# Kernel optimization log

Measured on AMD Instinct MI355X. Metric: run time of the kernel, lower is better.

Reference implementation:

```python
import jax, jax.numpy as jnp
import numpy as np

B, N, E = 16, 64, 512
C_IMG = 512
H1, H2, H3 = 256, 128, 64
U, R = 8, 8
BBC = 9
EH1, EH2 = 64, 64
BBOX_POS_MAX = 1024.0
EPS = 1e-5


def setup_inputs():
    key = jax.random.key(0)
    ks = jax.random.split(key, 24)
    f = lambda i, shape, s=0.05: jax.random.normal(ks[i], shape, jnp.float32) * s
    return {
        'roi_features': f(0, (B, N, C_IMG), 1.0),
        'batch_bboxes': jax.random.uniform(ks[1], (B, N, 4)) * BBOX_POS_MAX,
        'batch_directions': jax.random.uniform(ks[2], (B, N, 4)),
        'batch_priorities': jax.random.uniform(ks[3], (B, N)),
        'w1': f(4, (C_IMG, H1)), 'b1': f(5, (H1,)),
        'bn1_g': jnp.ones((H1,)), 'bn1_b': jnp.zeros((H1,)),
        'bn1_m': jnp.zeros((H1,)), 'bn1_v': jnp.ones((H1,)),
        'w2': f(6, (H1, H2)), 'b2': f(7, (H2,)),
        'bn2_g': jnp.ones((H2,)), 'bn2_b': jnp.zeros((H2,)),
        'bn2_m': jnp.zeros((H2,)), 'bn2_v': jnp.ones((H2,)),
        'w3': f(8, (H2, H3)), 'b3': f(9, (H3,)),
        'wn': f(10, (H3, U)), 'bn_c': f(11, (U,)),
        'we1': f(12, (2 * BBC, EH1)), 'be1': f(13, (EH1,)),
        'we2': f(14, (EH1, EH2)), 'be2': f(15, (EH2,)),
        'wei': f(16, (EH2, R)), 'bei': f(17, (R,)),
        'edge_index': jax.random.randint(ks[18], (B, 2, E), 0, N, dtype=jnp.int32),
    }


def _bn(x, g, b, m, v):
    # BatchNorm1d in eval mode (running stats)
    return (x - m) * jax.lax.rsqrt(v + EPS) * g + b


def _build_see(edge_index):
    # Padded neighbor table replacing edge_index2dict:
    # see[b,n,0] = n, then srcs of edges with dst==n, in original edge order.
    src = edge_index[:, 0, :]                                   # [B,E]
    dst = edge_index[:, 1, :]                                   # [B,E]
    eq = dst[:, :, None] == dst[:, None, :]                     # [B,E,E]
    lower = jnp.tril(jnp.ones((E, E), bool), -1)
    pos = jnp.sum(eq & lower, axis=-1) + 1                      # rank within dst group, +1 for self slot
    see = jnp.zeros((B, N, N), jnp.int32).at[:, :, 0].set(jnp.arange(N, dtype=jnp.int32))
    b_idx = jnp.arange(B)[:, None]
    see = see.at[b_idx, dst, pos].set(src, mode='drop')
    deg = jnp.zeros((B, N), jnp.int32).at[b_idx, dst].add(1)
    count = jnp.minimum(deg + 1, N)
    mask = (jnp.arange(N)[None, None, :] < count[:, :, None]).astype(jnp.float32)  # [B,N,N]
    return see, mask


def _forward(roi_features, batch_bboxes, batch_directions, batch_priorities,
             w1, b1, bn1_g, bn1_b, bn1_m, bn1_v,
             w2, b2, bn2_g, bn2_b, bn2_m, bn2_v,
             w3, b3, wn, bn_c,
             we1, be1, we2, be2, wei, bei, edge_index):
    see, mask = _build_see(edge_index)
    # --- node branch (node_predictor + node_concept_interpreter) ---
    x = roi_features.reshape(B * N, C_IMG)
    x = jax.nn.relu(_bn(x @ w1 + b1, bn1_g, bn1_b, bn1_m, bn1_v))
    x = jax.nn.relu(_bn(x @ w2 + b2, bn2_g, bn2_b, bn2_m, bn2_v))
    x = jax.nn.relu(x @ w3 + b3)
    node_c = jax.nn.sigmoid(x @ wn + bn_c).reshape(B, N, U)
    # get_nlm_unary_concepts: gather per-node neighborhood into dense [B,N,N,U]
    gu = jax.vmap(lambda u, s: u[s])(node_c, see)               # [B,N,N,U]
    node_concepts = (gu * mask[..., None]).reshape(B * N, N, U)
    # --- edge branch ---
    attr = jnp.concatenate([batch_bboxes / BBOX_POS_MAX, batch_directions,
                            batch_priorities[..., None]], axis=-1)  # [B,N,BBC]
    pair = jnp.concatenate([
        jnp.broadcast_to(attr[:, :, None, :], (B, N, N, BBC)),
        jnp.broadcast_to(attr[:, None, :, :], (B, N, N, BBC))], axis=-1).reshape(-1, 2 * BBC)
    e = jax.nn.relu(pair @ we1 + be1)
    e = jax.nn.relu(e @ we2 + be2)
    rel = jax.nn.sigmoid(e @ wei + bei).reshape(B, N, N, R)
    # get_nlm_binary_concepts: rel[b, see[b,n,i], see[b,n,j]] with zero padding
    def per_b(r, s, m):
        g = r[s[:, :, None], s[:, None, :]]                     # [N,N,N,R]
        return g * (m[:, :, None, None] * m[:, None, :, None])
    edge_concepts = jax.vmap(per_b)(rel, see, mask).reshape(B * N, N, N, R)
    return node_concepts, edge_concepts


def reference(roi_features, batch_bboxes, batch_directions, batch_priorities,
              w1, b1, bn1_g, bn1_b, bn1_m, bn1_v,
              w2, b2, bn2_g, bn2_b, bn2_m, bn2_v,
              w3, b3, wn, bn_c,
              we1, be1, we2, be2, wei, bei, edge_index):
    return _forward(roi_features, batch_bboxes, batch_directions, batch_priorities,
                    w1, b1, bn1_g, bn1_b, bn1_m, bn1_v,
                    w2, b2, bn2_g, bn2_b, bn2_m, bn2_v,
                    w3, b3, wn, bn_c,
                    we1, be1, we2, be2, wei, bei, edge_index)
```

## Files before the change

### kernel.cpp

```cpp
#include <hip/hip_runtime.h>
#include <math.h>

#define BB    16
#define NN    64
#define EE    512
#define CIMG  512
#define H1D   256
#define H2D   128
#define H3D   64
#define UD    8
#define RD    8
#define BBCD  9
#define EH1D  64
#define EH2D  64
#define EPSF  1e-5f

typedef float nfloat4 __attribute__((ext_vector_type(4)));

__global__ __launch_bounds__(256) void prep_node_kernel(
    const int* __restrict__ edge_index,
    const float* __restrict__ bboxes,
    const float* __restrict__ dirs,
    const float* __restrict__ prios,
    const float* __restrict__ we1,
    const float* __restrict__ be1,
    int* __restrict__ see, int* __restrict__ cnt,
    float* __restrict__ P, float* __restrict__ Q,
    const float* __restrict__ roi,
    const float* __restrict__ w1, const float* __restrict__ b1,
    const float* __restrict__ g1, const float* __restrict__ bt1,
    const float* __restrict__ m1, const float* __restrict__ v1,
    const float* __restrict__ w2, const float* __restrict__ b2,
    const float* __restrict__ g2, const float* __restrict__ bt2,
    const float* __restrict__ m2, const float* __restrict__ v2,
    const float* __restrict__ w3, const float* __restrict__ b3,
    const float* __restrict__ wn, const float* __restrict__ bnc,
    float* __restrict__ node_c)
{
    __shared__ union {
        struct {
            int src[EE];
            int dst[EE];
            int see[NN * NN];
            float attr[NN][BBCD];
        } p;
        struct {
            float h1[4][H1D];
            float h2[4][H2D];
            float h3[4][H3D];
        } n;
    } sm;

    const int t = threadIdx.x;

    if (blockIdx.x < BB) {
        const int b = blockIdx.x;
        const int* ei = edge_index + b * 2 * EE;
        for (int e = t; e < EE; e += 256) {
            sm.p.src[e] = ei[e];
            sm.p.dst[e] = ei[EE + e];
        }
        for (int x = t; x < NN * NN; x += 256)
            sm.p.see[x] = ((x & (NN - 1)) == 0) ? (x >> 6) : 0;
        if (t < NN) {
            const float* bbp = bboxes + (b * NN + t) * 4;
            const float* ddp = dirs + (b * NN + t) * 4;
            sm.p.attr[t][0] = bbp[0] * (1.0f / 1024.0f);
            sm.p.attr[t][1] = bbp[1] * (1.0f / 1024.0f);
            sm.p.attr[t][2] = bbp[2] * (1.0f / 1024.0f);
            sm.p.attr[t][3] = bbp[3] * (1.0f / 1024.0f);
            sm.p.attr[t][4] = ddp[0];
            sm.p.attr[t][5] = ddp[1];
            sm.p.attr[t][6] = ddp[2];
            sm.p.attr[t][7] = ddp[3];
            sm.p.attr[t][8] = prios[b * NN + t];
        }
        __syncthreads();

        if (t < NN) {
            int pos = 0;
            #pragma unroll 8
            for (int e = 0; e < EE; ++e) {
                if (sm.p.dst[e] == t) {
                    ++pos;
                    if (pos < NN) sm.p.see[t * NN + pos] = sm.p.src[e];
                }
            }
            int c = pos + 1;
            cnt[b * NN + t] = (c < NN) ? c : NN;
        }
        __syncthreads();

        {
            int4* dst4 = (int4*)(see + b * NN * NN);
            const int4* src4 = (const int4*)sm.p.see;
            for (int x = t; x < (NN * NN) / 4; x += 256) dst4[x] = src4[x];
        }

        for (int x = t; x < NN * EH1D; x += 256) {
            int n = x >> 6, o = x & 63;
            float p = 0.f;
            float q = be1[o];
            #pragma unroll
            for (int c = 0; c < BBCD; ++c) {
                float a = sm.p.attr[n][c];
                p = fmaf(a, we1[c * EH1D + o], p);
                q = fmaf(a, we1[(BBCD + c) * EH1D + o], q);
            }
            P[(b * NN + n) * EH1D + o] = p;
            Q[(b * NN + n) * EH1D + o] = q;
        }
        return;
    }

    const int row0 = (blockIdx.x - BB) * 4;

    {
        const int og = t & 63, rg = t >> 6;
        const int o0 = og * 4;
        const float4* xrow = (const float4*)(roi + (size_t)(row0 + rg) * CIMG);
        float a0 = 0.f, a1 = 0.f, a2 = 0.f, a3 = 0.f;
        for (int cg = 0; cg < CIMG / 4; ++cg) {
            float4 xv = xrow[cg];
            float4 wv0 = ((const float4*)(w1 + (size_t)(cg * 4 + 0) * H1D))[og];
            float4 wv1 = ((const float4*)(w1 + (size_t)(cg * 4 + 1) * H1D))[og];
            float4 wv2 = ((const float4*)(w1 + (size_t)(cg * 4 + 2) * H1D))[og];
            float4 wv3 = ((const float4*)(w1 + (size_t)(cg * 4 + 3) * H1D))[og];
            a0 = fmaf(xv.x, wv0.x, a0); a1 = fmaf(xv.x, wv0.y, a1);
            a2 = fmaf(xv.x, wv0.z, a2); a3 = fmaf(xv.x, wv0.w, a3);
            a0 = fmaf(xv.y, wv1.x, a0); a1 = fmaf(xv.y, wv1.y, a1);
            a2 = fmaf(xv.y, wv1.z, a2); a3 = fmaf(xv.y, wv1.w, a3);
            a0 = fmaf(xv.z, wv2.x, a0); a1 = fmaf(xv.z, wv2.y, a1);
            a2 = fmaf(xv.z, wv2.z, a2); a3 = fmaf(xv.z, wv2.w, a3);
            a0 = fmaf(xv.w, wv3.x, a0); a1 = fmaf(xv.w, wv3.y, a1);
            a2 = fmaf(xv.w, wv3.z, a2); a3 = fmaf(xv.w, wv3.w, a3);
        }
        float4 bv = ((const float4*)b1)[og];
        float4 gv = ((const float4*)g1)[og];
        float4 btv = ((const float4*)bt1)[og];
        float4 mv = ((const float4*)m1)[og];
        float4 vv = ((const float4*)v1)[og];
        float s0 = rsqrtf(vv.x + EPSF) * gv.x;
        float s1 = rsqrtf(vv.y + EPSF) * gv.y;
        float s2 = rsqrtf(vv.z + EPSF) * gv.z;
        float s3 = rsqrtf(vv.w + EPSF) * gv.w;
        sm.n.h1[rg][o0 + 0] = fmaxf(0.f, (a0 + bv.x - mv.x) * s0 + btv.x);
        sm.n.h1[rg][o0 + 1] = fmaxf(0.f, (a1 + bv.y - mv.y) * s1 + btv.y);
        sm.n.h1[rg][o0 + 2] = fmaxf(0.f, (a2 + bv.z - mv.z) * s2 + btv.z);
        sm.n.h1[rg][o0 + 3] = fmaxf(0.f, (a3 + bv.w - mv.w) * s3 + btv.w);
    }
    __syncthreads();

    if (t < 128) {
        const int og = t & 31, rg = t >> 5;
        const int o0 = og * 4;
        const float4* xrow = (const float4*)&sm.n.h1[rg][0];
        float a0 = 0.f, a1 = 0.f, a2 = 0.f, a3 = 0.f;
        for (int cg = 0; cg < H1D / 4; ++cg) {
            float4 xv = xrow[cg];
            float4 wv0 = ((const float4*)(w2 + (size_t)(cg * 4 + 0) * H2D))[og];
            float4 wv1 = ((const float4*)(w2 + (size_t)(cg * 4 + 1) * H2D))[og];
            float4 wv2 = ((const float4*)(w2 + (size_t)(cg * 4 + 2) * H2D))[og];
            float4 wv3 = ((const float4*)(w2 + (size_t)(cg * 4 + 3) * H2D))[og];
            a0 = fmaf(xv.x, wv0.x, a0); a1 = fmaf(xv.x, wv0.y, a1);
            a2 = fmaf(xv.x, wv0.z, a2); a3 = fmaf(xv.x, wv0.w, a3);
            a0 = fmaf(xv.y, wv1.x, a0); a1 = fmaf(xv.y, wv1.y, a1);
            a2 = fmaf(xv.y, wv1.z, a2); a3 = fmaf(xv.y, wv1.w, a3);
            a0 = fmaf(xv.z, wv2.x, a0); a1 = fmaf(xv.z, wv2.y, a1);
            a2 = fmaf(xv.z, wv2.z, a2); a3 = fmaf(xv.z, wv2.w, a3);
            a0 = fmaf(xv.w, wv3.x, a0); a1 = fmaf(xv.w, wv3.y, a1);
            a2 = fmaf(xv.w, wv3.z, a2); a3 = fmaf(xv.w, wv3.w, a3);
        }
        float4 bv = ((const float4*)b2)[og];
        float4 gv = ((const float4*)g2)[og];
        float4 btv = ((const float4*)bt2)[og];
        float4 mv = ((const float4*)m2)[og];
        float4 vv = ((const float4*)v2)[og];
        float s0 = rsqrtf(vv.x + EPSF) * gv.x;
        float s1 = rsqrtf(vv.y + EPSF) * gv.y;
        float s2 = rsqrtf(vv.z + EPSF) * gv.z;
        float s3 = rsqrtf(vv.w + EPSF) * gv.w;
        sm.n.h2[rg][o0 + 0] = fmaxf(0.f, (a0 + bv.x - mv.x) * s0 + btv.x);
        sm.n.h2[rg][o0 + 1] = fmaxf(0.f, (a1 + bv.y - mv.y) * s1 + btv.y);
        sm.n.h2[rg][o0 + 2] = fmaxf(0.f, (a2 + bv.z - mv.z) * s2 + btv.z);
        sm.n.h2[rg][o0 + 3] = fmaxf(0.f, (a3 + bv.w - mv.w) * s3 + btv.w);
    }
    __syncthreads();

    if (t < 64) {
        const int og = t & 15, rg = t >> 4;
        const int o0 = og * 4;
        const float4* xrow = (const float4*)&sm.n.h2[rg][0];
        float a0 = 0.f, a1 = 0.f, a2 = 0.f, a3 = 0.f;
        #pragma unroll 4
        for (int cg = 0; cg < H2D / 4; ++cg) {
            float4 xv = xrow[cg];
            float4 wv0 = ((const float4*)(w3 + (size_t)(cg * 4 + 0) * H3D))[og];
            float4 wv1 = ((const float4*)(w3 + (size_t)(cg * 4 + 1) * H3D))[og];
            float4 wv2 = ((const float4*)(w3 + (size_t)(cg * 4 + 2) * H3D))[og];
            float4 wv3 = ((const float4*)(w3 + (size_t)(cg * 4 + 3) * H3D))[og];
            a0 = fmaf(xv.x, wv0.x, a0); a1 = fmaf(xv.x, wv0.y, a1);
            a2 = fmaf(xv.x, wv0.z, a2); a3 = fmaf(xv.x, wv0.w, a3);
            a0 = fmaf(xv.y, wv1.x, a0); a1 = fmaf(xv.y, wv1.y, a1);
            a2 = fmaf(xv.y, wv1.z, a2); a3 = fmaf(xv.y, wv1.w, a3);
            a0 = fmaf(xv.z, wv2.x, a0); a1 = fmaf(xv.z, wv2.y, a1);
            a2 = fmaf(xv.z, wv2.z, a2); a3 = fmaf(xv.z, wv2.w, a3);
            a0 = fmaf(xv.w, wv3.x, a0); a1 = fmaf(xv.w, wv3.y, a1);
            a2 = fmaf(xv.w, wv3.z, a2); a3 = fmaf(xv.w, wv3.w, a3);
        }
        float4 bv = ((const float4*)b3)[og];
        sm.n.h3[rg][o0 + 0] = fmaxf(0.f, a0 + bv.x);
        sm.n.h3[rg][o0 + 1] = fmaxf(0.f, a1 + bv.y);
        sm.n.h3[rg][o0 + 2] = fmaxf(0.f, a2 + bv.z);
        sm.n.h3[rg][o0 + 3] = fmaxf(0.f, a3 + bv.w);
    }
    __syncthreads();

    if (t < 32) {
        const int o = t & 7, r = t >> 3;
        float a = bnc[o];
        #pragma unroll 8
        for (int c = 0; c < H3D; ++c) a = fmaf(sm.n.h3[r][c], wn[c * UD + o], a);
        node_c[(size_t)(row0 + r) * UD + o] = 1.f / (1.f + expf(-a));
    }
}

__global__ __launch_bounds__(256) void edge_zero_kernel(
    const float* __restrict__ P, const float* __restrict__ Q,
    const float* __restrict__ we2, const float* __restrict__ be2,
    const float* __restrict__ wei, const float* __restrict__ bei,
    const int* __restrict__ cnt,
    float* __restrict__ rel, float* __restrict__ out_edge)
{
    __shared__ float e1_s[NN * 68];
    __shared__ float qw_s[NN * EH1D];
    __shared__ float wei_s[EH2D * RD];
    __shared__ float Pi_s[EH1D];
    __shared__ float be2_s[EH2D];
    __shared__ float bei_s[RD];

    const int t = threadIdx.x;
    const int id = blockIdx.x >> 1;

    if ((blockIdx.x & 1) == 0) {
        const int c = cnt[id];
        float* outb = out_edge + (size_t)id * NN * NN * RD;
        const nfloat4 z = {0.f, 0.f, 0.f, 0.f};
        #pragma unroll
        for (int it = 0; it < (NN * NN) / 256; ++it) {
            int task = it * 256 + t;
            int j = task >> 6, k = task & 63;
            if (j >= c || k >= c) {
                nfloat4* dst = (nfloat4*)(outb + (size_t)task * RD);
                __builtin_nontemporal_store(z, dst);
                __builtin_nontemporal_store(z, dst + 1);
            }
        }
        return;
    }

    const int b = id >> 6;
    const int i = id & 63;

    {
        const float4* Qb4 = (const float4*)(Q + (size_t)b * NN * EH1D);
        float4* qw4 = (float4*)qw_s;
        #pragma unroll
        for (int x = 0; x < 4; ++x) qw4[x * 256 + t] = Qb4[x * 256 + t];
        if (t < EH1D) Pi_s[t] = P[(size_t)(b * NN + i) * EH1D + t];
        if (t < 128) ((float4*)wei_s)[t] = ((const float4*)wei)[t];
        if (t < EH2D) be2_s[t] = be2[t];
        if (t < RD) bei_s[t] = bei[t];
    }
    __syncthreads();

    {
        const int j = t & 63, cg = t >> 6;
        const float4* qrow = (const float4*)(qw_s + j * EH1D);
        const float4* prow = (const float4*)Pi_s;
        #pragma unroll
        for (int q = 0; q < 4; ++q) {
            int c4 = cg * 4 + q;
            float4 qv = qrow[c4];
            float4 pv = prow[c4];
            float4 ev;
            ev.x = fmaxf(0.f, qv.x + pv.x);
            ev.y = fmaxf(0.f, qv.y + pv.y);
            ev.z = fmaxf(0.f, qv.z + pv.z);
            ev.w = fmaxf(0.f, qv.w + pv.w);
            *(float4*)(e1_s + j * 68 + c4 * 4) = ev;
        }
    }
    __syncthreads();

    {
        const float4* w4 = (const float4*)we2;
        float4* qw4 = (float4*)qw_s;
        #pragma unroll
        for (int x = 0; x < 4; ++x) qw4[x * 256 + t] = w4[x * 256 + t];
    }
    __syncthreads();

    const int tx = t & 15, ty = t >> 4;
    const int o0 = tx * 4, j0 = ty * 4;
    float acc[4][4];
    #pragma unroll
    for (int r = 0; r < 4; ++r)
        #pragma unroll
        for (int o = 0; o < 4; ++o) acc[r][o] = 0.f;

    #pragma unroll 4
    for (int cg = 0; cg < 16; ++cg) {
        float ev[4][4];
        #pragma unroll
        for (int r = 0; r < 4; ++r) {
            float4 v = *(const float4*)(e1_s + (j0 + r) * 68 + cg * 4);
            ev[r][0] = v.x; ev[r][1] = v.y; ev[r][2] = v.z; ev[r][3] = v.w;
        }
        #pragma unroll
        for (int q = 0; q < 4; ++q) {
            float4 wv = *(const float4*)(qw_s + (cg * 4 + q) * EH1D + o0);
            #pragma unroll
            for (int r = 0; r < 4; ++r) {
                acc[r][0] = fmaf(ev[r][q], wv.x, acc[r][0]);
                acc[r][1] = fmaf(ev[r][q], wv.y, acc[r][1]);
                acc[r][2] = fmaf(ev[r][q], wv.z, acc[r][2]);
                acc[r][3] = fmaf(ev[r][q], wv.w, acc[r][3]);
            }
        }
    }

    {
        float4 bv = *(const float4*)(be2_s + o0);
        #pragma unroll
        for (int r = 0; r < 4; ++r) {
            float4 v;
            v.x = fmaxf(0.f, acc[r][0] + bv.x);
            v.y = fmaxf(0.f, acc[r][1] + bv.y);
            v.z = fmaxf(0.f, acc[r][2] + bv.z);
            v.w = fmaxf(0.f, acc[r][3] + bv.w);
            *(float4*)(e1_s + (j0 + r) * 68 + o0) = v;
        }
    }
    __syncthreads();

    {
        const int j = t >> 2;
        const int r0 = (t & 3) * 2;
        float a0 = bei_s[r0], a1 = bei_s[r0 + 1];
        const float* e2row = e1_s + j * 68;
        #pragma unroll
        for (int og = 0; og < 16; ++og) {
            float4 e2v = *(const float4*)(e2row + og * 4);
            float2 w0 = *(const float2*)(wei_s + (og * 4 + 0) * RD + r0);
            float2 w1 = *(const float2*)(wei_s + (og * 4 + 1) * RD + r0);
            float2 w2 = *(const float2*)(wei_s + (og * 4 + 2) * RD + r0);
            float2 w3 = *(const float2*)(wei_s + (og * 4 + 3) * RD + r0);
            a0 = fmaf(e2v.x, w0.x, a0); a1 = fmaf(e2v.x, w0.y, a1);
            a0 = fmaf(e2v.y, w1.x, a0); a1 = fmaf(e2v.y, w1.y, a1);
            a0 = fmaf(e2v.z, w2.x, a0); a1 = fmaf(e2v.z, w2.y, a1);
            a0 = fmaf(e2v.w, w3.x, a0); a1 = fmaf(e2v.w, w3.y, a1);
        }
        float2 o;
        o.x = 1.f / (1.f + expf(-a0));
        o.y = 1.f / (1.f + expf(-a1));
        *(float2*)(rel + ((size_t)(b * NN + i) * NN + j) * RD + r0) = o;
    }
}

__global__ __launch_bounds__(256) void gather_kernel(
    const int* __restrict__ see, const int* __restrict__ cnt,
    const float* __restrict__ node_c, const float* __restrict__ rel,
    float* __restrict__ out_node, float* __restrict__ out_edge)
{
    __shared__ int s_s[NN];

    const int t = threadIdx.x;
    const int bi = blockIdx.x;
    const int b = bi >> 6;
    const int c = cnt[bi];

    if (t < NN) s_s[t] = see[bi * NN + t];
    __syncthreads();

    if (t < NN) {
        const float m = (t < c) ? 1.f : 0.f;
        const float4* src = (const float4*)(node_c + (size_t)(b * NN + s_s[t]) * UD);
        float4 v0 = src[0], v1 = src[1];
        v0.x *= m; v0.y *= m; v0.z *= m; v0.w *= m;
        v1.x *= m; v1.y *= m; v1.z *= m; v1.w *= m;
        float4* dst = (float4*)(out_node + ((size_t)bi * NN + t) * UD);
        dst[0] = v0;
        dst[1] = v1;
    }

    const float* relb = rel + (size_t)b * NN * NN * RD;
    float* outb = out_edge + (size_t)bi * NN * NN * RD;

    const int total = c * c;
    for (int task = t; task < total; task += 256) {
        int j = task / c;
        int k = task - j * c;
        const float4* src =
            (const float4*)(relb + (size_t)(s_s[j] * NN + s_s[k]) * RD);
        float4 v0 = src[0], v1 = src[1];
        float4* dst = (float4*)(outb + ((size_t)j * NN + k) * RD);
        dst[0] = v0;
        dst[1] = v1;
    }
}

extern "C" void kernel_launch(void* const* d_in, const int* in_sizes, int n_in,
                              void* d_out, int out_size, void* d_ws, size_t ws_size,
                              hipStream_t stream)
{
    const float* roi  = (const float*)d_in[0];
    const float* bbox = (const float*)d_in[1];
    const float* dirs = (const float*)d_in[2];
    const float* prio = (const float*)d_in[3];
    const float* w1   = (const float*)d_in[4];
    const float* b1   = (const float*)d_in[5];
    const float* g1   = (const float*)d_in[6];
    const float* bt1  = (const float*)d_in[7];
    const float* m1   = (const float*)d_in[8];
    const float* v1   = (const float*)d_in[9];
    const float* w2   = (const float*)d_in[10];
    const float* b2   = (const float*)d_in[11];
    const float* g2   = (const float*)d_in[12];
    const float* bt2  = (const float*)d_in[13];
    const float* m2   = (const float*)d_in[14];
    const float* v2   = (const float*)d_in[15];
    const float* w3   = (const float*)d_in[16];
    const float* b3   = (const float*)d_in[17];
    const float* wn   = (const float*)d_in[18];
    const float* bnc  = (const float*)d_in[19];
    const float* we1  = (const float*)d_in[20];
    const float* be1  = (const float*)d_in[21];
    const float* we2  = (const float*)d_in[22];
    const float* be2  = (const float*)d_in[23];
    const float* wei  = (const float*)d_in[24];
    const float* bei  = (const float*)d_in[25];
    const int* edge_index = (const int*)d_in[26];

    char* ws = (char*)d_ws;
    int*   see    = (int*)ws;   ws += (size_t)BB * NN * NN * 4;
    int*   cnt    = (int*)ws;   ws += (size_t)BB * NN * 4;
    float* Pbuf   = (float*)ws; ws += (size_t)BB * NN * EH1D * 4;
    float* Qbuf   = (float*)ws; ws += (size_t)BB * NN * EH1D * 4;
    float* node_c = (float*)ws; ws += (size_t)BB * NN * UD * 4;
    float* rel    = (float*)ws; ws += (size_t)BB * NN * NN * RD * 4;

    float* out_node = (float*)d_out;
    float* out_edge = (float*)d_out + (size_t)BB * NN * NN * UD;

    hipLaunchKernelGGL(prep_node_kernel, dim3(BB + 256), dim3(256), 0, stream,
                       edge_index, bbox, dirs, prio, we1, be1,
                       see, cnt, Pbuf, Qbuf,
                       roi, w1, b1, g1, bt1, m1, v1,
                       w2, b2, g2, bt2, m2, v2,
                       w3, b3, wn, bnc, node_c);
    hipLaunchKernelGGL(edge_zero_kernel, dim3(2 * BB * NN), dim3(256), 0, stream,
                       Pbuf, Qbuf, we2, be2, wei, bei, cnt, rel, out_edge);
    hipLaunchKernelGGL(gather_kernel, dim3(BB * NN), dim3(256), 0, stream,
                       see, cnt, node_c, rel, out_node, out_edge);
}
```

Measured before the change: 283.7 us.

## Register-tile node MLP with split-K reduction and move edge zeroing into first kernel

The node MLP layers now use 4x4 register tiles per thread with split-K partial sums reduced through shared memory. This replaces the previous scheme in which many threads sat idle in the later layers and each weight load fed only one row. The output-edge zero fill moves out of the edge MLP kernel into extra blocks of the first kernel and now clears the whole tensor unconditionally instead of only the masked region. That lets it overlap with the node work, but it writes more bytes, relies on the gather kernel overwriting the valid entries, and enlarges the shared-memory union.

```diff
diff --git a/kernel.cpp b/kernel.cpp
--- a/kernel.cpp
+++ b/kernel.cpp
@@ -17,7 +17,7 @@
 
 typedef float nfloat4 __attribute__((ext_vector_type(4)));
 
-__global__ __launch_bounds__(256) void prep_node_kernel(
+__global__ __launch_bounds__(256) void fused1_kernel(
     const int* __restrict__ edge_index,
     const float* __restrict__ bboxes,
     const float* __restrict__ dirs,
@@ -35,7 +35,8 @@
     const float* __restrict__ m2, const float* __restrict__ v2,
     const float* __restrict__ w3, const float* __restrict__ b3,
     const float* __restrict__ wn, const float* __restrict__ bnc,
-    float* __restrict__ node_c)
+    float* __restrict__ node_c,
+    float* __restrict__ out_edge)
 {
     __shared__ union {
         struct {
@@ -45,6 +46,7 @@
             float attr[NN][BBCD];
         } p;
         struct {
+            float part[4096];
             float h1[4][H1D];
             float h2[4][H2D];
             float h3[4][H3D];
@@ -52,6 +54,19 @@
     } sm;
 
     const int t = threadIdx.x;
+
+    if (blockIdx.x >= BB + 256) {
+        const int id = blockIdx.x - (BB + 256);
+        nfloat4* dst = (nfloat4*)(out_edge + (size_t)id * NN * NN * RD);
+        const nfloat4 z = {0.f, 0.f, 0.f, 0.f};
+        #pragma unroll
+        for (int it = 0; it < 16; ++it) {
+            int task = it * 256 + t;
+            __builtin_nontemporal_store(z, dst + task * 2);
+            __builtin_nontemporal_store(z, dst + task * 2 + 1);
+        }
+        return;
+    }
 
     if (blockIdx.x < BB) {
         const int b = blockIdx.x;
@@ -114,105 +129,162 @@
     }
 
     const int row0 = (blockIdx.x - BB) * 4;
-
-    {
-        const int og = t & 63, rg = t >> 6;
-        const int o0 = og * 4;
-        const float4* xrow = (const float4*)(roi + (size_t)(row0 + rg) * CIMG);
-        float a0 = 0.f, a1 = 0.f, a2 = 0.f, a3 = 0.f;
-        for (int cg = 0; cg < CIMG / 4; ++cg) {
-            float4 xv = xrow[cg];
-            float4 wv0 = ((const float4*)(w1 + (size_t)(cg * 4 + 0) * H1D))[og];
-            float4 wv1 = ((const float4*)(w1 + (size_t)(cg * 4 + 1) * H1D))[og];
-            float4 wv2 = ((const float4*)(w1 + (size_t)(cg * 4 + 2) * H1D))[og];
-            float4 wv3 = ((const float4*)(w1 + (size_t)(cg * 4 + 3) * H1D))[og];
-            a0 = fmaf(xv.x, wv0.x, a0); a1 = fmaf(xv.x, wv0.y, a1);
-            a2 = fmaf(xv.x, wv0.z, a2); a3 = fmaf(xv.x, wv0.w, a3);
-            a0 = fmaf(xv.y, wv1.x, a0); a1 = fmaf(xv.y, wv1.y, a1);
-            a2 = fmaf(xv.y, wv1.z, a2); a3 = fmaf(xv.y, wv1.w, a3);
-            a0 = fmaf(xv.z, wv2.x, a0); a1 = fmaf(xv.z, wv2.y, a1);
-            a2 = fmaf(xv.z, wv2.z, a2); a3 = fmaf(xv.z, wv2.w, a3);
-            a0 = fmaf(xv.w, wv3.x, a0); a1 = fmaf(xv.w, wv3.y, a1);
-            a2 = fmaf(xv.w, wv3.z, a2); a3 = fmaf(xv.w, wv3.w, a3);
-        }
-        float4 bv = ((const float4*)b1)[og];
-        float4 gv = ((const float4*)g1)[og];
-        float4 btv = ((const float4*)bt1)[og];
-        float4 mv = ((const float4*)m1)[og];
-        float4 vv = ((const float4*)v1)[og];
-        float s0 = rsqrtf(vv.x + EPSF) * gv.x;
-        float s1 = rsqrtf(vv.y + EPSF) * gv.y;
-        float s2 = rsqrtf(vv.z + EPSF) * gv.z;
-        float s3 = rsqrtf(vv.w + EPSF) * gv.w;
-        sm.n.h1[rg][o0 + 0] = fmaxf(0.f, (a0 + bv.x - mv.x) * s0 + btv.x);
-        sm.n.h1[rg][o0 + 1] = fmaxf(0.f, (a1 + bv.y - mv.y) * s1 + btv.y);
-        sm.n.h1[rg][o0 + 2] = fmaxf(0.f, (a2 + bv.z - mv.z) * s2 + btv.z);
-        sm.n.h1[rg][o0 + 3] = fmaxf(0.f, (a3 + bv.w - mv.w) * s3 + btv.w);
-    }
-    __syncthreads();
-
-    if (t < 128) {
-        const int og = t & 31, rg = t >> 5;
-        const int o0 = og * 4;
-        const float4* xrow = (const float4*)&sm.n.h1[rg][0];
-        float a0 = 0.f, a1 = 0.f, a2 = 0.f, a3 = 0.f;
-        for (int cg = 0; cg < H1D / 4; ++cg) {
-            float4 xv = xrow[cg];
-            float4 wv0 = ((const float4*)(w2 + (size_t)(cg * 4 + 0) * H2D))[og];
-            float4 wv1 = ((const float4*)(w2 + (size_t)(cg * 4 + 1) * H2D))[og];
-            float4 wv2 = ((const float4*)(w2 + (size_t)(cg * 4 + 2) * H2D))[og];
-            float4 wv3 = ((const float4*)(w2 + (size_t)(cg * 4 + 3) * H2D))[og];
-            a0 = fmaf(xv.x, wv0.x, a0); a1 = fmaf(xv.x, wv0.y, a1);
-            a2 = fmaf(xv.x, wv0.z, a2); a3 = fmaf(xv.x, wv0.w, a3);
-            a0 = fmaf(xv.y, wv1.x, a0); a1 = fmaf(xv.y, wv1.y, a1);
-            a2 = fmaf(xv.y, wv1.z, a2); a3 = fmaf(xv.y, wv1.w, a3);
-            a0 = fmaf(xv.z, wv2.x, a0); a1 = fmaf(xv.z, wv2.y, a1);
-            a2 = fmaf(xv.z, wv2.z, a2); a3 = fmaf(xv.z, wv2.w, a3);
-            a0 = fmaf(xv.w, wv3.x, a0); a1 = fmaf(xv.w, wv3.y, a1);
-            a2 = fmaf(xv.w, wv3.z, a2); a3 = fmaf(xv.w, wv3.w, a3);
-        }
-        float4 bv = ((const float4*)b2)[og];
-        float4 gv = ((const float4*)g2)[og];
-        float4 btv = ((const float4*)bt2)[og];
-        float4 mv = ((const float4*)m2)[og];
-        float4 vv = ((const float4*)v2)[og];
-        float s0 = rsqrtf(vv.x + EPSF) * gv.x;
-        float s1 = rsqrtf(vv.y + EPSF) * gv.y;
-        float s2 = rsqrtf(vv.z + EPSF) * gv.z;
-        float s3 = rsqrtf(vv.w + EPSF) * gv.w;
-        sm.n.h2[rg][o0 + 0] = fmaxf(0.f, (a0 + bv.x - mv.x) * s0 + btv.x);
-        sm.n.h2[rg][o0 + 1] = fmaxf(0.f, (a1 + bv.y - mv.y) * s1 + btv.y);
-        sm.n.h2[rg][o0 + 2] = fmaxf(0.f, (a2 + bv.z - mv.z) * s2 + btv.z);
-        sm.n.h2[rg][o0 + 3] = fmaxf(0.f, (a3 + bv.w - mv.w) * s3 + btv.w);
-    }
-    __syncthreads();
-
-    if (t < 64) {
-        const int og = t & 15, rg = t >> 4;
-        const int o0 = og * 4;
-        const float4* xrow = (const float4*)&sm.n.h2[rg][0];
-        float a0 = 0.f, a1 = 0.f, a2 = 0.f, a3 = 0.f;
-        #pragma unroll 4
-        for (int cg = 0; cg < H2D / 4; ++cg) {
-            float4 xv = xrow[cg];
-            float4 wv0 = ((const float4*)(w3 + (size_t)(cg * 4 + 0) * H3D))[og];
-            float4 wv1 = ((const float4*)(w3 + (size_t)(cg * 4 + 1) * H3D))[og];
-            float4 wv2 = ((const float4*)(w3 + (size_t)(cg * 4 + 2) * H3D))[og];
-            float4 wv3 = ((const float4*)(w3 + (size_t)(cg * 4 + 3) * H3D))[og];
-            a0 = fmaf(xv.x, wv0.x, a0); a1 = fmaf(xv.x, wv0.y, a1);
-            a2 = fmaf(xv.x, wv0.z, a2); a3 = fmaf(xv.x, wv0.w, a3);
-            a0 = fmaf(xv.y, wv1.x, a0); a1 = fmaf(xv.y, wv1.y, a1);
-            a2 = fmaf(xv.y, wv1.z, a2); a3 = fmaf(xv.y, wv1.w, a3);
-            a0 = fmaf(xv.z, wv2.x, a0); a1 = fmaf(xv.z, wv2.y, a1);
-            a2 = fmaf(xv.z, wv2.z, a2); a3 = fmaf(xv.z, wv2.w, a3);
-            a0 = fmaf(xv.w, wv3.x, a0); a1 = fmaf(xv.w, wv3.y, a1);
-            a2 = fmaf(xv.w, wv3.z, a2); a3 = fmaf(xv.w, wv3.w, a3);
-        }
-        float4 bv = ((const float4*)b3)[og];
-        sm.n.h3[rg][o0 + 0] = fmaxf(0.f, a0 + bv.x);
-        sm.n.h3[rg][o0 + 1] = fmaxf(0.f, a1 + bv.y);
-        sm.n.h3[rg][o0 + 2] = fmaxf(0.f, a2 + bv.z);
-        sm.n.h3[rg][o0 + 3] = fmaxf(0.f, a3 + bv.w);
+    float* part = sm.n.part;
+
+    {
+        const int og = t & 63, kg = t >> 6;
+        const float4* w1v = (const float4*)w1;
+        const float4* roiv = (const float4*)(roi + (size_t)row0 * CIMG);
+        float acc[4][4];
+        #pragma unroll
+        for (int r = 0; r < 4; ++r)
+            #pragma unroll
+            for (int c = 0; c < 4; ++c) acc[r][c] = 0.f;
+
+        for (int cq = 0; cq < 32; ++cq) {
+            const int c4 = kg * 32 + cq;
+            float x[4][4], w[4][4];
+            #pragma unroll
+            for (int r = 0; r < 4; ++r) {
+                float4 v = roiv[r * 128 + c4];
+                x[r][0] = v.x; x[r][1] = v.y; x[r][2] = v.z; x[r][3] = v.w;
+            }
+            #pragma unroll
+            for (int q = 0; q < 4; ++q) {
+                float4 v = w1v[(size_t)(c4 * 4 + q) * 64 + og];
+                w[q][0] = v.x; w[q][1] = v.y; w[q][2] = v.z; w[q][3] = v.w;
+            }
+            #pragma unroll
+            for (int r = 0; r < 4; ++r)
+                #pragma unroll
+                for (int q = 0; q < 4; ++q)
+                    #pragma unroll
+                    for (int c = 0; c < 4; ++c)
+                        acc[r][c] = fmaf(x[r][q], w[q][c], acc[r][c]);
+        }
+        #pragma unroll
+        for (int r = 0; r < 4; ++r) {
+            float4 v = {acc[r][0], acc[r][1], acc[r][2], acc[r][3]};
+            *(float4*)(part + (kg * 4 + r) * 256 + og * 4) = v;
+        }
+    }
+    __syncthreads();
+    {
+        const int o = t;
+        const float bias = b1[o];
+        const float scale = rsqrtf(v1[o] + EPSF) * g1[o];
+        const float beta = bt1[o];
+        const float mu = m1[o];
+        #pragma unroll
+        for (int r = 0; r < 4; ++r) {
+            float s = part[(0 * 4 + r) * 256 + o] + part[(1 * 4 + r) * 256 + o]
+                    + part[(2 * 4 + r) * 256 + o] + part[(3 * 4 + r) * 256 + o];
+            sm.n.h1[r][o] = fmaxf(0.f, (s + bias - mu) * scale + beta);
+        }
+    }
+    __syncthreads();
+
+    {
+        const int og = t & 31, kg = t >> 5;
+        const float4* w2v = (const float4*)w2;
+        float acc[4][4];
+        #pragma unroll
+        for (int r = 0; r < 4; ++r)
+            #pragma unroll
+            for (int c = 0; c < 4; ++c) acc[r][c] = 0.f;
+
+        #pragma unroll
+        for (int cq = 0; cq < 8; ++cq) {
+            const int c4 = kg * 8 + cq;
+            float x[4][4], w[4][4];
+            #pragma unroll
+            for (int r = 0; r < 4; ++r) {
+                float4 v = *(const float4*)&sm.n.h1[r][c4 * 4];
+                x[r][0] = v.x; x[r][1] = v.y; x[r][2] = v.z; x[r][3] = v.w;
+            }
+            #pragma unroll
+            for (int q = 0; q < 4; ++q) {
+                float4 v = w2v[(size_t)(c4 * 4 + q) * 32 + og];
+                w[q][0] = v.x; w[q][1] = v.y; w[q][2] = v.z; w[q][3] = v.w;
+            }
+            #pragma unroll
+            for (int r = 0; r < 4; ++r)
+                #pragma unroll
+                for (int q = 0; q < 4; ++q)
+                    #pragma unroll
+                    for (int c = 0; c < 4; ++c)
+                        acc[r][c] = fmaf(x[r][q], w[q][c], acc[r][c]);
+        }
+        #pragma unroll
+        for (int r = 0; r < 4; ++r) {
+            float4 v = {acc[r][0], acc[r][1], acc[r][2], acc[r][3]};
+            *(float4*)(part + (kg * 4 + r) * 128 + og * 4) = v;
+        }
+    }
+    __syncthreads();
+    {
+        const int o = t & 127;
+        const int rp = t >> 7;
+        const float bias = b2[o];
+        const float scale = rsqrtf(v2[o] + EPSF) * g2[o];
+        const float beta = bt2[o];
+        const float mu = m2[o];
+        #pragma unroll
+        for (int rr = 0; rr < 2; ++rr) {
+            const int r = rp + rr * 2;
+            float s = 0.f;
+            #pragma unroll
+            for (int kg = 0; kg < 8; ++kg) s += part[(kg * 4 + r) * 128 + o];
+            sm.n.h2[r][o] = fmaxf(0.f, (s + bias - mu) * scale + beta);
+        }
+    }
+    __syncthreads();
+
+    {
+        const int og = t & 15, kg = t >> 4;
+        const float4* w3v = (const float4*)w3;
+        float acc[4][4];
+        #pragma unroll
+        for (int r = 0; r < 4; ++r)
+            #pragma unroll
+            for (int c = 0; c < 4; ++c) acc[r][c] = 0.f;
+
+        #pragma unroll
+        for (int cq = 0; cq < 2; ++cq) {
+            const int c4 = kg * 2 + cq;
+            float x[4][4], w[4][4];
+            #pragma unroll
+            for (int r = 0; r < 4; ++r) {
+                float4 v = *(const float4*)&sm.n.h2[r][c4 * 4];
+                x[r][0] = v.x; x[r][1] = v.y; x[r][2] = v.z; x[r][3] = v.w;
+            }
+            #pragma unroll
+            for (int q = 0; q < 4; ++q) {
+                float4 v = w3v[(size_t)(c4 * 4 + q) * 16 + og];
+                w[q][0] = v.x; w[q][1] = v.y; w[q][2] = v.z; w[q][3] = v.w;
+            }
+            #pragma unroll
+            for (int r = 0; r < 4; ++r)
+                #pragma unroll
+                for (int q = 0; q < 4; ++q)
+                    #pragma unroll
+                    for (int c = 0; c < 4; ++c)
+                        acc[r][c] = fmaf(x[r][q], w[q][c], acc[r][c]);
+        }
+        #pragma unroll
+        for (int r = 0; r < 4; ++r) {
+            float4 v = {acc[r][0], acc[r][1], acc[r][2], acc[r][3]};
+            *(float4*)(part + (kg * 4 + r) * 64 + og * 4) = v;
+        }
+    }
+    __syncthreads();
+    {
+        const int o = t & 63;
+        const int r = t >> 6;
+        float s = b3[o];
+        #pragma unroll
+        for (int kg = 0; kg < 16; ++kg) s += part[(kg * 4 + r) * 64 + o];
+        sm.n.h3[r][o] = fmaxf(0.f, s);
     }
     __syncthreads();
 
@@ -225,12 +297,11 @@
     }
 }
 
-__global__ __launch_bounds__(256) void edge_zero_kernel(
+__global__ __launch_bounds__(256) void edge_mlp_kernel(
     const float* __restrict__ P, const float* __restrict__ Q,
     const float* __restrict__ we2, const float* __restrict__ be2,
     const float* __restrict__ wei, const float* __restrict__ bei,
-    const int* __restrict__ cnt,
-    float* __restrict__ rel, float* __restrict__ out_edge)
+    float* __restrict__ rel)
 {
     __shared__ float e1_s[NN * 68];
     __shared__ float qw_s[NN * EH1D];
@@ -240,27 +311,8 @@
     __shared__ float bei_s[RD];
 
     const int t = threadIdx.x;
-    const int id = blockIdx.x >> 1;
-
-    if ((blockIdx.x & 1) == 0) {
-        const int c = cnt[id];
-        float* outb = out_edge + (size_t)id * NN * NN * RD;
-        const nfloat4 z = {0.f, 0.f, 0.f, 0.f};
-        #pragma unroll
-        for (int it = 0; it < (NN * NN) / 256; ++it) {
-            int task = it * 256 + t;
-            int j = task >> 6, k = task & 63;
-            if (j >= c || k >= c) {
-                nfloat4* dst = (nfloat4*)(outb + (size_t)task * RD);
-                __builtin_nontemporal_store(z, dst);
-                __builtin_nontemporal_store(z, dst + 1);
-            }
-        }
-        return;
-    }
-
-    const int b = id >> 6;
-    const int i = id & 63;
+    const int b = blockIdx.x >> 6;
+    const int i = blockIdx.x & 63;
 
     {
         const float4* Qb4 = (const float4*)(Q + (size_t)b * NN * EH1D);
@@ -453,14 +505,14 @@
     float* out_node = (float*)d_out;
     float* out_edge = (float*)d_out + (size_t)BB * NN * NN * UD;
 
-    hipLaunchKernelGGL(prep_node_kernel, dim3(BB + 256), dim3(256), 0, stream,
+    hipLaunchKernelGGL(fused1_kernel, dim3(BB + 256 + BB * NN), dim3(256), 0, stream,
                        edge_index, bbox, dirs, prio, we1, be1,
                        see, cnt, Pbuf, Qbuf,
                        roi, w1, b1, g1, bt1, m1, v1,
                        w2, b2, g2, bt2, m2, v2,
-                       w3, b3, wn, bnc, node_c);
-    hipLaunchKernelGGL(edge_zero_kernel, dim3(2 * BB * NN), dim3(256), 0, stream,
-                       Pbuf, Qbuf, we2, be2, wei, bei, cnt, rel, out_edge);
+                       w3, b3, wn, bnc, node_c, out_edge);
+    hipLaunchKernelGGL(edge_mlp_kernel, dim3(BB * NN), dim3(256), 0, stream,
+                       Pbuf, Qbuf, we2, be2, wei, bei, rel);
     hipLaunchKernelGGL(gather_kernel, dim3(BB * NN), dim3(256), 0, stream,
                        see, cnt, node_c, rel, out_node, out_edge);
 }
```

New measurement: 250.6 us (median of 2 runs). -11.7%, faster.
